# Kernel tuning notes

Hardware: AMD Instinct MI355X
Metric: run time of the kernel (lower is better)

The kernel has to match this reference:

```python
import jax, jax.numpy as jnp
import numpy as np

VOCAB, H, MAXLEN = 50257, 1024, 128


def setup_inputs() -> dict:
    key = jax.random.key(0)
    ks = jax.random.split(key, 14)
    s = 0.02  # init scale
    f32 = jnp.float32
    return {
        "x": jax.random.randint(ks[0], (1,), 0, VOCAB),
        "h": jax.random.normal(ks[1], (1, 1, H), f32),
        "encoder_outputs": jax.random.normal(ks[2], (MAXLEN, H), f32),
        "emb": jax.random.normal(ks[3], (VOCAB, H), f32) * s,
        "W_attn": jax.random.normal(ks[4], (MAXLEN, 2 * H), f32) * s,
        "b_attn": jnp.zeros((MAXLEN,), f32),
        "W_comb": jax.random.normal(ks[5], (H, 2 * H), f32) * s,
        "b_comb": jnp.zeros((H,), f32),
        "w_ih": jax.random.normal(ks[6], (3 * H, H), f32) * s,
        "w_hh": jax.random.normal(ks[7], (3 * H, H), f32) * s,
        "b_ih": jnp.zeros((3 * H,), f32),
        "b_hh": jnp.zeros((3 * H,), f32),
        "W_out": jax.random.normal(ks[8], (VOCAB, H), f32) * s,
        "b_out": jnp.zeros((VOCAB,), f32),
    }


def reference(x, h, encoder_outputs, emb, W_attn, b_attn, W_comb, b_comb,
              w_ih, w_hh, b_ih, b_hh, W_out, b_out):
    # Single decode step (batch=1, seq=1); dropout in eval mode (identity).
    e = emb[x]                       # [1, H] embedded token
    h0 = h[0]                        # [1, H] hidden state
    # attention over encoder outputs
    attn_w = jax.nn.softmax(jnp.concatenate([e, h0], axis=1) @ W_attn.T + b_attn, axis=1)  # [1, MAXLEN]
    attn_applied = attn_w @ encoder_outputs                                                 # [1, H]
    # combine + relu
    g = jax.nn.relu(jnp.concatenate([e, attn_applied], axis=1) @ W_comb.T + b_comb)        # [1, H]
    # single-step GRU (PyTorch gate order: r, z, n)
    gi = g @ w_ih.T + b_ih           # [1, 3H]
    gh = h0 @ w_hh.T + b_hh          # [1, 3H]
    i_r, i_z, i_n = jnp.split(gi, 3, axis=1)
    h_r, h_z, h_n = jnp.split(gh, 3, axis=1)
    r = jax.nn.sigmoid(i_r + h_r)
    z = jax.nn.sigmoid(i_z + h_z)
    n = jnp.tanh(i_n + r * h_n)
    h_new = (1.0 - z) * n + z * h0   # [1, H]
    out = jax.nn.log_softmax(h_new @ W_out.T + b_out, axis=1)  # [1, VOCAB]
    return out, h_new[None], attn_w
```

## Files before the change

### kernel.cpp

```cpp
#include <hip/hip_runtime.h>
#include <hip/hip_bf16.h>
#include <math.h>

#define H 1024
#define MAXLEN 128
#define VOCAB 50257

__device__ inline float wave_reduce_sum(float v) {
    #pragma unroll
    for (int off = 32; off > 0; off >>= 1) v += __shfl_down(v, off);
    return v;
}

__global__ void k_attn_logits(const int* x, const float* h, const float* emb,
                              const float* W_attn, const float* b_attn, float* logits) {
    const int row = blockIdx.x;
    const float* w = W_attn + row * (2 * H);
    const float* e = emb + (long long)x[0] * H;
    float acc = 0.f;
    for (int k = threadIdx.x; k < 2 * H; k += blockDim.x) {
        float c = (k < H) ? e[k] : h[k - H];
        acc += c * w[k];
    }
    __shared__ float red[4];
    int lane = threadIdx.x & 63, wid = threadIdx.x >> 6;
    acc = wave_reduce_sum(acc);
    if (lane == 0) red[wid] = acc;
    __syncthreads();
    if (threadIdx.x == 0)
        logits[row] = red[0] + red[1] + red[2] + red[3] + b_attn[row];
}

__global__ void k_softmax128(const float* logits, float* attn_w, float* out_attn) {
    __shared__ float red[MAXLEN];
    int t = threadIdx.x;
    float v = logits[t];
    red[t] = v;
    __syncthreads();
    for (int s = 64; s > 0; s >>= 1) { if (t < s) red[t] = fmaxf(red[t], red[t + s]); __syncthreads(); }
    float m = red[0];
    __syncthreads();
    float ex = expf(v - m);
    red[t] = ex;
    __syncthreads();
    for (int s = 64; s > 0; s >>= 1) { if (t < s) red[t] += red[t + s]; __syncthreads(); }
    float w = ex / red[0];
    attn_w[t] = w;
    out_attn[t] = w;
}

__global__ void k_attn_apply(const float* attn_w, const float* enc, float* out) {
    __shared__ float w[MAXLEN];
    if (threadIdx.x < MAXLEN) w[threadIdx.x] = attn_w[threadIdx.x];
    __syncthreads();
    int j = blockIdx.x * blockDim.x + threadIdx.x;
    float acc = 0.f;
    #pragma unroll 8
    for (int k = 0; k < MAXLEN; k++) acc += w[k] * enc[k * H + j];
    out[j] = acc;
}

__global__ void k_combine(const int* x, const float* emb, const float* attn_applied,
                          const float* W_comb, const float* b_comb, float* g) {
    int wid = threadIdx.x >> 6, lane = threadIdx.x & 63;
    int row = blockIdx.x * 4 + wid;
    const float4* w4 = (const float4*)(W_comb + (long long)row * (2 * H));
    const float4* e4 = (const float4*)(emb + (long long)x[0] * H);
    const float4* a4 = (const float4*)attn_applied;
    float acc = 0.f;
    #pragma unroll
    for (int i = 0; i < 8; i++) {
        int idx = lane + i * 64;
        float4 wv = w4[idx];
        float4 cv = (idx < 256) ? e4[idx] : a4[idx - 256];
        acc += wv.x * cv.x + wv.y * cv.y + wv.z * cv.z + wv.w * cv.w;
    }
    acc = wave_reduce_sum(acc);
    if (lane == 0) g[row] = fmaxf(acc + b_comb[row], 0.f);
}

__global__ void k_gru_mm(const float* g, const float* h,
                         const float* w_ih, const float* w_hh,
                         const float* b_ih, const float* b_hh,
                         float* gi, float* gh) {
    int wid = threadIdx.x >> 6, lane = threadIdx.x & 63;
    int gRow = blockIdx.x * 4 + wid;
    const float* vec;
    const float* mat;
    const float* bias;
    float* out;
    int row;
    if (gRow < 3 * H) { row = gRow; vec = g; mat = w_ih; bias = b_ih; out = gi; }
    else { row = gRow - 3 * H; vec = h; mat = w_hh; bias = b_hh; out = gh; }
    const float4* w4 = (const float4*)(mat + (long long)row * H);
    const float4* v4 = (const float4*)vec;
    float acc = 0.f;
    #pragma unroll
    for (int i = 0; i < 4; i++) {
        int idx = lane + i * 64;
        float4 wv = w4[idx];
        float4 vv = v4[idx];
        acc += wv.x * vv.x + wv.y * vv.y + wv.z * vv.z + wv.w * vv.w;
    }
    acc = wave_reduce_sum(acc);
    if (lane == 0) out[row] = acc + bias[row];
}

__global__ void k_gates(const float* gi, const float* gh, const float* h, float* h_new) {
    int j = threadIdx.x;
    float r = 1.f / (1.f + expf(-(gi[j] + gh[j])));
    float z = 1.f / (1.f + expf(-(gi[j + H] + gh[j + H])));
    float n = tanhf(gi[j + 2 * H] + r * gh[j + 2 * H]);
    h_new[j] = (1.f - z) * n + z * h[j];
}

__global__ void k_out_matvec(const float* hn, const float* W_out, const float* b_out, float* out) {
    int wid = threadIdx.x >> 6, lane = threadIdx.x & 63;
    int row = blockIdx.x * 4 + wid;
    if (row >= VOCAB) return;
    const float4* w4 = (const float4*)(W_out + (long long)row * H);
    const float4* h4 = (const float4*)hn;
    float acc = 0.f;
    #pragma unroll
    for (int i = 0; i < 4; i++) {
        int idx = lane + i * 64;
        float4 wv = w4[idx];
        float4 hv = h4[idx];
        acc += wv.x * hv.x + wv.y * hv.y + wv.z * hv.z + wv.w * hv.w;
    }
    acc = wave_reduce_sum(acc);
    if (lane == 0) out[row] = acc + b_out[row];
}

__global__ void k_lse(const float* out, float* c) {
    __shared__ float red[16];
    __shared__ float Msh;
    int lane = threadIdx.x & 63, wid = threadIdx.x >> 6;
    float m = -1e30f;
    for (int i = threadIdx.x; i < VOCAB; i += blockDim.x) m = fmaxf(m, out[i]);
    #pragma unroll
    for (int off = 32; off > 0; off >>= 1) m = fmaxf(m, __shfl_down(m, off));
    if (lane == 0) red[wid] = m;
    __syncthreads();
    if (threadIdx.x == 0) {
        float mm = red[0];
        for (int i = 1; i < 16; i++) mm = fmaxf(mm, red[i]);
        Msh = mm;
    }
    __syncthreads();
    float M = Msh;
    float s = 0.f;
    for (int i = threadIdx.x; i < VOCAB; i += blockDim.x) s += expf(out[i] - M);
    s = wave_reduce_sum(s);
    if (lane == 0) red[wid] = s;
    __syncthreads();
    if (threadIdx.x == 0) {
        float ss = 0.f;
        for (int i = 0; i < 16; i++) ss += red[i];
        c[0] = M + logf(ss);
    }
}

__global__ void k_sub(float* out, const float* c) {
    int v = blockIdx.x * blockDim.x + threadIdx.x;
    if (v < VOCAB) out[v] -= c[0];
}

extern "C" void kernel_launch(void* const* d_in, const int* in_sizes, int n_in,
                              void* d_out, int out_size, void* d_ws, size_t ws_size,
                              hipStream_t stream) {
    const int*   x     = (const int*)d_in[0];
    const float* h     = (const float*)d_in[1];
    const float* enc   = (const float*)d_in[2];
    const float* emb   = (const float*)d_in[3];
    const float* W_attn= (const float*)d_in[4];
    const float* b_attn= (const float*)d_in[5];
    const float* W_comb= (const float*)d_in[6];
    const float* b_comb= (const float*)d_in[7];
    const float* w_ih  = (const float*)d_in[8];
    const float* w_hh  = (const float*)d_in[9];
    const float* b_ih  = (const float*)d_in[10];
    const float* b_hh  = (const float*)d_in[11];
    const float* W_out = (const float*)d_in[12];
    const float* b_out = (const float*)d_in[13];

    float* out      = (float*)d_out;
    float* out_h    = out + VOCAB;
    float* out_attn = out + VOCAB + H;

    float* ws       = (float*)d_ws;
    float* logits128   = ws;
    float* attn_w      = ws + 128;
    float* attn_applied= ws + 256;
    float* g           = ws + 1280;
    float* gi          = ws + 2304;
    float* gh          = ws + 5376;
    float* lse_c       = ws + 8448;

    k_attn_logits<<<MAXLEN, 256, 0, stream>>>(x, h, emb, W_attn, b_attn, logits128);
    k_softmax128<<<1, MAXLEN, 0, stream>>>(logits128, attn_w, out_attn);
    k_attn_apply<<<H / 256, 256, 0, stream>>>(attn_w, enc, attn_applied);
    k_combine<<<H / 4, 256, 0, stream>>>(x, emb, attn_applied, W_comb, b_comb, g);
    k_gru_mm<<<(6 * H) / 4, 256, 0, stream>>>(g, h, w_ih, w_hh, b_ih, b_hh, gi, gh);
    k_gates<<<1, H, 0, stream>>>(gi, gh, h, out_h);
    k_out_matvec<<<(VOCAB + 3) / 4, 256, 0, stream>>>(out_h, W_out, b_out, out);
    k_lse<<<1, 1024, 0, stream>>>(out, lse_c);
    k_sub<<<(VOCAB + 255) / 256, 256, 0, stream>>>(out, lse_c);
}
```

Measured before the change: 84.14 us.

## Fuse attention softmax into apply and compute per-block log-sum-exp partials

The 128-way softmax is folded into the attention-apply kernel, so each block recomputes the max and sum redundantly and one launch is removed. The output matvec now writes a per-block max and exp-sum, and the single-block LSE kernel merges about 12.5K partials instead of rescanning 50K logits twice. The attention-logits kernel switches to float4 loads. The cost is redundant softmax work in each apply block and extra workspace for the partials.

```diff
diff --git a/kernel.cpp b/kernel.cpp
--- a/kernel.cpp
+++ b/kernel.cpp
@@ -5,6 +5,7 @@
 #define H 1024
 #define MAXLEN 128
 #define VOCAB 50257
+#define NB_OUT ((VOCAB + 3) / 4)
 
 __device__ inline float wave_reduce_sum(float v) {
     #pragma unroll
@@ -15,49 +16,49 @@
 __global__ void k_attn_logits(const int* x, const float* h, const float* emb,
                               const float* W_attn, const float* b_attn, float* logits) {
     const int row = blockIdx.x;
-    const float* w = W_attn + row * (2 * H);
-    const float* e = emb + (long long)x[0] * H;
-    float acc = 0.f;
-    for (int k = threadIdx.x; k < 2 * H; k += blockDim.x) {
-        float c = (k < H) ? e[k] : h[k - H];
-        acc += c * w[k];
+    const float4* w4 = (const float4*)(W_attn + row * (2 * H));
+    const float4* e4 = (const float4*)(emb + (long long)x[0] * H);
+    const float4* h4 = (const float4*)h;
+    float acc = 0.f;
+    int t = threadIdx.x;
+    #pragma unroll
+    for (int i = 0; i < 2; i++) {
+        int idx = t + i * 256;
+        float4 wv = w4[idx];
+        float4 cv = (idx < 256) ? e4[idx] : h4[idx - 256];
+        acc += wv.x * cv.x + wv.y * cv.y + wv.z * cv.z + wv.w * cv.w;
     }
     __shared__ float red[4];
-    int lane = threadIdx.x & 63, wid = threadIdx.x >> 6;
+    int lane = t & 63, wid = t >> 6;
     acc = wave_reduce_sum(acc);
     if (lane == 0) red[wid] = acc;
     __syncthreads();
-    if (threadIdx.x == 0)
+    if (t == 0)
         logits[row] = red[0] + red[1] + red[2] + red[3] + b_attn[row];
 }
 
-__global__ void k_softmax128(const float* logits, float* attn_w, float* out_attn) {
-    __shared__ float red[MAXLEN];
+__global__ void k_attn_sm_apply(const float* logits, const float* enc,
+                                float* attn_applied, float* out_attn) {
+    __shared__ float buf[MAXLEN];
+    __shared__ float w[MAXLEN];
     int t = threadIdx.x;
-    float v = logits[t];
-    red[t] = v;
-    __syncthreads();
-    for (int s = 64; s > 0; s >>= 1) { if (t < s) red[t] = fmaxf(red[t], red[t + s]); __syncthreads(); }
-    float m = red[0];
-    __syncthreads();
-    float ex = expf(v - m);
-    red[t] = ex;
-    __syncthreads();
-    for (int s = 64; s > 0; s >>= 1) { if (t < s) red[t] += red[t + s]; __syncthreads(); }
-    float w = ex / red[0];
-    attn_w[t] = w;
-    out_attn[t] = w;
-}
-
-__global__ void k_attn_apply(const float* attn_w, const float* enc, float* out) {
-    __shared__ float w[MAXLEN];
-    if (threadIdx.x < MAXLEN) w[threadIdx.x] = attn_w[threadIdx.x];
-    __syncthreads();
-    int j = blockIdx.x * blockDim.x + threadIdx.x;
+    if (t < MAXLEN) buf[t] = logits[t];
+    __syncthreads();
+    float m = -INFINITY;
+    #pragma unroll 8
+    for (int k = 0; k < MAXLEN; k++) m = fmaxf(m, buf[k]);
+    if (t < MAXLEN) w[t] = expf(buf[t] - m);
+    __syncthreads();
+    float s = 0.f;
+    #pragma unroll 8
+    for (int k = 0; k < MAXLEN; k++) s += w[k];
+    float inv = 1.f / s;
+    int j = blockIdx.x * blockDim.x + t;
     float acc = 0.f;
     #pragma unroll 8
     for (int k = 0; k < MAXLEN; k++) acc += w[k] * enc[k * H + j];
-    out[j] = acc;
+    attn_applied[j] = acc * inv;
+    if (blockIdx.x == 0 && t < MAXLEN) out_attn[t] = w[t] * inv;
 }
 
 __global__ void k_combine(const int* x, const float* emb, const float* attn_applied,
@@ -114,30 +115,45 @@
     h_new[j] = (1.f - z) * n + z * h[j];
 }
 
-__global__ void k_out_matvec(const float* hn, const float* W_out, const float* b_out, float* out) {
+__global__ void k_out_matvec(const float* hn, const float* W_out, const float* b_out,
+                             float* out, float* pmax, float* psum) {
     int wid = threadIdx.x >> 6, lane = threadIdx.x & 63;
     int row = blockIdx.x * 4 + wid;
-    if (row >= VOCAB) return;
-    const float4* w4 = (const float4*)(W_out + (long long)row * H);
-    const float4* h4 = (const float4*)hn;
-    float acc = 0.f;
-    #pragma unroll
-    for (int i = 0; i < 4; i++) {
-        int idx = lane + i * 64;
-        float4 wv = w4[idx];
-        float4 hv = h4[idx];
-        acc += wv.x * hv.x + wv.y * hv.y + wv.z * hv.z + wv.w * hv.w;
-    }
-    acc = wave_reduce_sum(acc);
-    if (lane == 0) out[row] = acc + b_out[row];
-}
-
-__global__ void k_lse(const float* out, float* c) {
+    __shared__ float lm[4];
+    float logit = -INFINITY;
+    if (row < VOCAB) {
+        const float4* w4 = (const float4*)(W_out + (long long)row * H);
+        const float4* h4 = (const float4*)hn;
+        float acc = 0.f;
+        #pragma unroll
+        for (int i = 0; i < 4; i++) {
+            int idx = lane + i * 64;
+            float4 wv = w4[idx];
+            float4 hv = h4[idx];
+            acc += wv.x * hv.x + wv.y * hv.y + wv.z * hv.z + wv.w * hv.w;
+        }
+        acc = wave_reduce_sum(acc);
+        if (lane == 0) { logit = acc + b_out[row]; out[row] = logit; }
+    }
+    if (lane == 0) lm[wid] = logit;
+    __syncthreads();
+    if (threadIdx.x == 0) {
+        float m = fmaxf(fmaxf(lm[0], lm[1]), fmaxf(lm[2], lm[3]));
+        float s = 0.f;
+        #pragma unroll
+        for (int i = 0; i < 4; i++)
+            if (lm[i] != -INFINITY) s += expf(lm[i] - m);
+        pmax[blockIdx.x] = m;
+        psum[blockIdx.x] = s;
+    }
+}
+
+__global__ void k_lse_merge(const float* pmax, const float* psum, float* c) {
     __shared__ float red[16];
     __shared__ float Msh;
     int lane = threadIdx.x & 63, wid = threadIdx.x >> 6;
-    float m = -1e30f;
-    for (int i = threadIdx.x; i < VOCAB; i += blockDim.x) m = fmaxf(m, out[i]);
+    float m = -INFINITY;
+    for (int i = threadIdx.x; i < NB_OUT; i += blockDim.x) m = fmaxf(m, pmax[i]);
     #pragma unroll
     for (int off = 32; off > 0; off >>= 1) m = fmaxf(m, __shfl_down(m, off));
     if (lane == 0) red[wid] = m;
@@ -150,7 +166,7 @@
     __syncthreads();
     float M = Msh;
     float s = 0.f;
-    for (int i = threadIdx.x; i < VOCAB; i += blockDim.x) s += expf(out[i] - M);
+    for (int i = threadIdx.x; i < NB_OUT; i += blockDim.x) s += psum[i] * expf(pmax[i] - M);
     s = wave_reduce_sum(s);
     if (lane == 0) red[wid] = s;
     __syncthreads();
@@ -190,20 +206,20 @@
 
     float* ws       = (float*)d_ws;
     float* logits128   = ws;
-    float* attn_w      = ws + 128;
     float* attn_applied= ws + 256;
     float* g           = ws + 1280;
     float* gi          = ws + 2304;
     float* gh          = ws + 5376;
     float* lse_c       = ws + 8448;
+    float* pmax        = ws + 9216;
+    float* psum        = ws + 22272;
 
     k_attn_logits<<<MAXLEN, 256, 0, stream>>>(x, h, emb, W_attn, b_attn, logits128);
-    k_softmax128<<<1, MAXLEN, 0, stream>>>(logits128, attn_w, out_attn);
-    k_attn_apply<<<H / 256, 256, 0, stream>>>(attn_w, enc, attn_applied);
+    k_attn_sm_apply<<<H / 256, 256, 0, stream>>>(logits128, enc, attn_applied, out_attn);
     k_combine<<<H / 4, 256, 0, stream>>>(x, emb, attn_applied, W_comb, b_comb, g);
     k_gru_mm<<<(6 * H) / 4, 256, 0, stream>>>(g, h, w_ih, w_hh, b_ih, b_hh, gi, gh);
     k_gates<<<1, H, 0, stream>>>(gi, gh, h, out_h);
-    k_out_matvec<<<(VOCAB + 3) / 4, 256, 0, stream>>>(out_h, W_out, b_out, out);
-    k_lse<<<1, 1024, 0, stream>>>(out, lse_c);
+    k_out_matvec<<<NB_OUT, 256, 0, stream>>>(out_h, W_out, b_out, out, pmax, psum);
+    k_lse_merge<<<1, 1024, 0, stream>>>(pmax, psum, lse_c);
     k_sub<<<(VOCAB + 255) / 256, 256, 0, stream>>>(out, lse_c);
 }
```

New measurement: 74.12 us. -11.9%, faster.
